# Performance work log

Measured on AMD Instinct MI355X. Metric: run time of the kernel, lower is better.

The kernel has to match this reference:

```python
import jax, jax.numpy as jnp
import numpy as np

B, N_REL, N_OBJ, N_ATT, VOCAB, D = 32, 1024, 1024, 4, 2048, 512


def setup_inputs() -> dict:
    key = jax.random.key(0)
    ks = jax.random.split(key, 12)
    inp = {}
    inp["ssg_rel"] = jax.random.randint(ks[0], (B, N_REL, 3), 0, N_OBJ, dtype=jnp.int32)
    inp["ssg_obj"] = jax.random.randint(ks[1], (B, N_OBJ), 0, VOCAB, dtype=jnp.int32)
    inp["ssg_att"] = jax.random.randint(ks[2], (B, N_OBJ, N_ATT), 0, VOCAB, dtype=jnp.int32)
    inp["emb_table"] = jax.random.normal(ks[3], (VOCAB, D), jnp.float32) * 0.02
    def lin(k, fan_in):
        return jax.random.normal(k, (fan_in, D), jnp.float32) * (1.0 / np.sqrt(fan_in))
    inp["W_sbj"] = lin(ks[4], 3 * D); inp["b_sbj"] = jnp.zeros((D,), jnp.float32)
    inp["W_obj"] = lin(ks[5], 3 * D); inp["b_obj"] = jnp.zeros((D,), jnp.float32)
    inp["W_rel"] = lin(ks[6], 3 * D); inp["b_rel"] = jnp.zeros((D,), jnp.float32)
    inp["W_o"] = lin(ks[7], D);      inp["b_o"] = jnp.zeros((D,), jnp.float32)
    inp["W_a"] = lin(ks[8], 2 * D);  inp["b_a"] = jnp.zeros((D,), jnp.float32)
    return inp


def reference(ssg_rel, ssg_obj, ssg_att, emb_table,
              W_sbj, b_sbj, W_obj, b_obj, W_rel, b_rel, W_o, b_o, W_a, b_a):
    # Dropout is identity in eval mode.
    Bq, N_rel, _ = ssg_rel.shape
    _, N_obj, N_att = ssg_att.shape
    d = emb_table.shape[1]

    rel_mask = (ssg_rel[:, :, 2] == 1)[..., None]      # [B, N_rel, 1], True = pad
    obj_mask = ssg_obj == 1                            # [B, N_obj]
    attr_mask = ssg_att == 1                           # [B, N_obj, N_att]

    rel_emb = emb_table[ssg_rel[:, :, 2]]              # [B, N_rel, d]
    obj_emb = emb_table[ssg_obj]                       # [B, N_obj, d]
    attr_emb = emb_table[ssg_att]                      # [B, N_obj, N_att, d]

    sbj_id = ssg_rel[:, :, 0]
    obj_id = ssg_rel[:, :, 1]
    gather = lambda ids: jnp.take_along_axis(obj_emb, ids[..., None], axis=1)  # [B,N_rel,d]
    sbj_g = gather(sbj_id)
    obj_g = gather(obj_id)

    zfill = lambda x: jnp.where(rel_mask, 0.0, x)
    # Sequential overwriting matches the original: rel_obj/rel_rel use the UPDATED sbj/obj feats.
    sbj_f = zfill(jax.nn.relu(jnp.concatenate([sbj_g, obj_g, rel_emb], -1) @ W_sbj + b_sbj))
    obj_f = zfill(jax.nn.relu(jnp.concatenate([sbj_f, obj_g, rel_emb], -1) @ W_obj + b_obj))
    rel_f = zfill(jax.nn.relu(jnp.concatenate([sbj_f, obj_f, rel_emb], -1) @ W_rel + b_rel))

    node = jnp.where(obj_mask[..., None], 0.0, jax.nn.relu(obj_emb @ W_o + b_o))  # [B,N_obj,d]

    att_in = jnp.concatenate(
        [jnp.broadcast_to(obj_emb[:, :, None, :], (Bq, N_obj, N_att, d)), attr_emb], -1)
    att_f = jnp.where(attr_mask[..., None], 0.0, jax.nn.relu(att_in @ W_a + b_a))  # [B,N_obj,N_att,d]

    bidx = jnp.arange(Bq)[:, None]
    node = node.at[bidx, sbj_id].add(sbj_f)
    node = node.at[bidx, obj_id].add(obj_f)

    # Original builds counts=ones(B, 2*N_rel, N_obj+1) then scatters 1s into it -> a no-op,
    # so counts.sum(dim=1) == 2*N_rel everywhere; the divisor is the constant 2*N_rel.
    rel_object_feat = node / jnp.asarray(2.0 * N_rel, node.dtype)

    att_sum = att_f.sum(axis=2)                        # [B, N_obj, d]
    att_cnt = jnp.sum(~attr_mask, axis=-1)             # [B, N_obj] number of valid attrs
    attr_zero = att_cnt == 0
    denom = jnp.maximum(att_cnt, 1).astype(att_sum.dtype)[..., None]
    att_feat = jnp.where(attr_zero[..., None], 0.0, att_sum / denom)

    ssg_feat = jnp.concatenate([rel_object_feat, rel_f, att_feat], axis=1)
    ssg_mask = jnp.concatenate([obj_mask, rel_mask[..., 0], attr_zero], axis=1)[:, None, None, :]
    return ssg_feat, ssg_mask
```

## Files before the change

kernel.cpp:

```cpp
#include <hip/hip_runtime.h>
#include <hip/hip_bf16.h>

typedef __attribute__((ext_vector_type(8))) short bf16x8;
typedef __attribute__((ext_vector_type(4))) float f32x4;

#define N_OBJ 1024
#define N_REL 1024
#define NB 32
#define D 512
#define VOCAB 2048
#define M_ROWS (NB * N_REL)
#define PRE_BLK (VOCAB * D)
#define WT_BLK (D * D)

__device__ __forceinline__ ushort f2bf(float f) {
    union { float f; unsigned u; } v; v.f = f;
    unsigned u = v.u;
    unsigned r = (u + 0x7FFFu + ((u >> 16) & 1u)) >> 16;
    return (ushort)r;
}
__device__ __forceinline__ float bf2f(ushort h) {
    union { unsigned u; float f; } v; v.u = ((unsigned)h) << 16;
    return v.f;
}

__device__ __forceinline__ void gload16(const ushort* g, const ushort* l) {
    __builtin_amdgcn_global_load_lds(
        (const __attribute__((address_space(1))) void*)(unsigned long long)(const void*)g,
        (__attribute__((address_space(3))) void*)(unsigned)(unsigned long long)(const void*)l,
        16, 0, 0);
}

template <int MODE>
__device__ __forceinline__ void gemm_body(
    int mt, int nt, int q, int tid,
    ushort* __restrict__ sA, ushort* __restrict__ sB,
    const ushort* __restrict__ A, const ushort* __restrict__ WT,
    ushort* __restrict__ PREB,
    const int* __restrict__ ssg_rel, const int* __restrict__ ssg_obj,
    const float* __restrict__ bias,
    ushort* __restrict__ featbuf, float* __restrict__ out0,
    float* __restrict__ out1) {
    const int m0 = mt * 128;
    constexpr int LDA = (MODE == 0) ? 512 : 1024;
    constexpr int KTOT = (MODE == 2) ? 1024 : 512;

    const ushort* BT0;
    const ushort* BT1 = nullptr;
    ushort* PREq = nullptr;
    if (MODE == 0) {
        const int wtq[9] = {0, 1, 2, 4, 5, 8, 9, 10, 11};
        BT0 = WT + (size_t)wtq[q] * WT_BLK + (size_t)nt * 128 * 512;
        PREq = PREB + (size_t)q * PRE_BLK;
    } else if (MODE == 1) {
        BT0 = WT + (size_t)3 * WT_BLK + (size_t)nt * 128 * 512;
    } else {
        BT0 = WT + (size_t)6 * WT_BLK + (size_t)nt * 128 * 512;
        BT1 = WT + (size_t)7 * WT_BLK + (size_t)nt * 128 * 512;
    }

    const int wave = tid >> 6;
    const int wm = wave >> 1, wn = wave & 1;
    const int lr = tid & 15, lk = (tid & 63) >> 4;

    f32x4 acc[4][4];
#pragma unroll
    for (int mi = 0; mi < 4; mi++)
#pragma unroll
        for (int ni = 0; ni < 4; ni++)
            acc[mi][ni] = (f32x4){0.f, 0.f, 0.f, 0.f};

    const ushort* Ag = A + (size_t)m0 * LDA;
    const int srow = tid >> 3;
    const int scol = (tid & 7) * 8;

    for (int k0 = 0; k0 < KTOT; k0 += 64) {
        const ushort* As = Ag + (size_t)srow * LDA + k0 + scol;
        const ushort* Bbase = (MODE == 2 && k0 >= 512) ? (BT1 + (k0 - 512)) : (BT0 + k0);
        const ushort* Bs = Bbase + (size_t)srow * 512 + scol;
#pragma unroll
        for (int i = 0; i < 4; i++)
            gload16(As + (size_t)i * 32 * LDA, &sA[i * 2048 + tid * 8]);
#pragma unroll
        for (int i = 0; i < 4; i++)
            gload16(Bs + (size_t)i * 32 * 512, &sB[i * 2048 + tid * 8]);
        __syncthreads();
#pragma unroll
        for (int ks = 0; ks < 2; ks++) {
            bf16x8 af[4], bfr[4];
#pragma unroll
            for (int mi = 0; mi < 4; mi++)
                af[mi] = *(const bf16x8*)&sA[(wm * 64 + mi * 16 + lr) * 64 + ks * 32 + lk * 8];
#pragma unroll
            for (int ni = 0; ni < 4; ni++)
                bfr[ni] = *(const bf16x8*)&sB[(wn * 64 + ni * 16 + lr) * 64 + ks * 32 + lk * 8];
#pragma unroll
            for (int mi = 0; mi < 4; mi++)
#pragma unroll
                for (int ni = 0; ni < 4; ni++)
                    acc[mi][ni] = __builtin_amdgcn_mfma_f32_16x16x32_bf16(af[mi], bfr[ni], acc[mi][ni], 0, 0, 0);
        }
        __syncthreads();
    }

    int* sIo  = (int*)sA;
    int* sRid = sIo + 128;
    if (MODE == 1 || MODE == 2) {
        if (tid < 128) {
            int R = m0 + tid;
            int rid = ssg_rel[R * 3 + 2];
            sRid[tid] = rid;
            if (MODE == 1) sIo[tid] = ssg_obj[(R & ~(N_OBJ - 1)) + ssg_rel[R * 3 + 1]];
            if (MODE == 2 && nt == 0) {
                int b = R >> 10, rr = R & (N_REL - 1);
                out1[(size_t)b * 3072 + 1024 + rr] = (rid == 1) ? 1.0f : 0.0f;
            }
        }
        __syncthreads();
    }

#pragma unroll
    for (int mi = 0; mi < 4; mi++) {
#pragma unroll
        for (int ni = 0; ni < 4; ni++) {
            int c = wn * 64 + ni * 16 + lr;
            int ch = nt * 128 + c;
#pragma unroll
            for (int j = 0; j < 4; j++) {
                int rl = wm * 64 + mi * 16 + lk * 4 + j;
                int R = m0 + rl;
                float v = acc[mi][ni][j];
                if (MODE == 0) {
                    PREq[(size_t)R * 512 + ch] = f2bf(v);
                } else if (MODE == 1) {
                    int rid = sRid[rl];
                    int io = sIo[rl];
                    float t = v + bf2f(PREB[(size_t)3 * PRE_BLK + (size_t)io * 512 + ch])
                                + bf2f(PREB[(size_t)4 * PRE_BLK + (size_t)rid * 512 + ch])
                                + bias[ch];
                    t = fmaxf(t, 0.f);
                    if (rid == 1) t = 0.f;
                    featbuf[(size_t)R * 1024 + 512 + ch] = f2bf(t);
                } else {
                    int rid = sRid[rl];
                    float t = v + bf2f(PREB[(size_t)5 * PRE_BLK + (size_t)rid * 512 + ch])
                                + bias[ch];
                    t = fmaxf(t, 0.f);
                    if (rid == 1) t = 0.f;
                    int b = R >> 10, rr = R & (N_REL - 1);
                    out0[((size_t)(b * 3072 + 1024 + rr)) * 512 + ch] = t;
                }
            }
        }
    }
}

__global__ __launch_bounds__(256)
void k_setup(const float* __restrict__ E, ushort* __restrict__ EB,
             const float* __restrict__ Wsbj, const float* __restrict__ Wobj,
             const float* __restrict__ Wrel, const float* __restrict__ Wo,
             const float* __restrict__ Wa, ushort* __restrict__ WT,
             int* __restrict__ cnt) {
    int blk = blockIdx.x, tid = threadIdx.x;
    if (blk < 1024) {
        int i = blk * 256 + tid;
        float4 v = ((const float4*)E)[i];
        ushort4 o; o.x = f2bf(v.x); o.y = f2bf(v.y); o.z = f2bf(v.z); o.w = f2bf(v.w);
        ((ushort4*)EB)[i] = o;
    } else if (blk < 4096) {
        __shared__ float s[32][33];
        int bb = blk - 1024;
        int q = bb >> 8, rem = bb & 255;
        int bx = rem & 15, by = rem >> 4;
        const float* src; int ro;
        if (q < 3)       { src = Wsbj; ro = q * 512; }
        else if (q < 6)  { src = Wobj; ro = (q - 3) * 512; }
        else if (q < 9)  { src = Wrel; ro = (q - 6) * 512; }
        else if (q == 9) { src = Wo;   ro = 0; }
        else             { src = Wa;   ro = (q - 10) * 512; }
        int tx = tid & 31, ty = tid >> 5;
        int kbase = by * 32, nbase = bx * 32;
#pragma unroll
        for (int i = 0; i < 4; i++) {
            int k = kbase + ty + i * 8;
            s[ty + i * 8][tx] = src[(size_t)(ro + k) * 512 + nbase + tx];
        }
        __syncthreads();
        ushort* dst = WT + (size_t)q * WT_BLK;
#pragma unroll
        for (int i = 0; i < 4; i++) {
            int n = nbase + ty + i * 8;
            dst[(size_t)n * 512 + kbase + tx] = f2bf(s[tx][ty + i * 8]);
        }
    } else {
        cnt[(blk - 4096) * 256 + tid] = 0;
    }
}

__global__ void k_csr_count(const int* __restrict__ ssg_rel, int* __restrict__ cnt) {
    int r = blockIdx.x * 256 + threadIdx.x;
    int bb = r & ~(N_OBJ - 1);
    atomicAdd(&cnt[bb + ssg_rel[r * 3 + 0]], 1);
    atomicAdd(&cnt[bb + ssg_rel[r * 3 + 1]], 1);
}

__global__ __launch_bounds__(1024)
void k_csr_scan(const int* __restrict__ cnt, int* __restrict__ offs, int* __restrict__ cursor) {
    __shared__ int part[1024];
    int t = threadIdx.x;
    int base = t * 32;
    int local[32];
    int sum = 0;
#pragma unroll
    for (int i = 0; i < 32; i++) { local[i] = sum; sum += cnt[base + i]; }
    part[t] = sum;
    __syncthreads();
    for (int d = 1; d < 1024; d <<= 1) {
        int v = (t >= d) ? part[t - d] : 0;
        __syncthreads();
        part[t] += v;
        __syncthreads();
    }
    int excl = (t == 0) ? 0 : part[t - 1];
#pragma unroll
    for (int i = 0; i < 32; i++) {
        int o = excl + local[i];
        offs[base + i] = o;
        cursor[base + i] = o;
    }
    if (t == 1023) offs[32768] = part[1023];
}

__global__ __launch_bounds__(256)
void k_pre_fill(const ushort* __restrict__ EB, const ushort* __restrict__ WT,
                ushort* __restrict__ PREB, const int* __restrict__ ssg_rel,
                int* __restrict__ cursor, int* __restrict__ lists) {
    int blk = blockIdx.x, tid = threadIdx.x;
    if (blk < 576) {
        int q = blk >> 6, mt = (blk >> 2) & 15, nt = blk & 3;
        if ((q == 2 || q == 4 || q == 5) && mt >= 8) return;
        __shared__ __attribute__((aligned(16))) ushort sA[128 * 64];
        __shared__ __attribute__((aligned(16))) ushort sB[128 * 64];
        gemm_body<0>(mt, nt, q, tid, sA, sB, EB, WT, PREB,
                     nullptr, nullptr, nullptr, nullptr, nullptr, nullptr);
    } else {
        int r = (blk - 576) * 256 + tid;
        int bb = r & ~(N_OBJ - 1);
        int p0 = atomicAdd(&cursor[bb + ssg_rel[r * 3 + 0]], 1);
        lists[p0] = r * 2;
        int p1 = atomicAdd(&cursor[bb + ssg_rel[r * 3 + 1]], 1);
        lists[p1] = r * 2 + 1;
    }
}

__global__ void k_sbj(const int* __restrict__ ssg_rel, const int* __restrict__ ssg_obj,
                      const ushort* __restrict__ PREB, const float* __restrict__ b_sbj,
                      ushort* __restrict__ featbuf) {
    int R = blockIdx.x * 2 + (threadIdx.x >> 7);
    int c4 = threadIdx.x & 127;
    int sid = ssg_rel[R * 3 + 0];
    int oid = ssg_rel[R * 3 + 1];
    int rid = ssg_rel[R * 3 + 2];
    int bb = R & ~(N_OBJ - 1);
    int is_ = ssg_obj[bb + sid];
    int io  = ssg_obj[bb + oid];
    ushort4 p1 = ((const ushort4*)(PREB + (size_t)is_ * 512))[c4];
    ushort4 p2 = ((const ushort4*)(PREB + (size_t)1 * PRE_BLK + (size_t)io * 512))[c4];
    ushort4 p3 = ((const ushort4*)(PREB + (size_t)2 * PRE_BLK + (size_t)rid * 512))[c4];
    float4 b  = ((const float4*)b_sbj)[c4];
    float4 v;
    v.x = fmaxf(bf2f(p1.x) + bf2f(p2.x) + bf2f(p3.x) + b.x, 0.f);
    v.y = fmaxf(bf2f(p1.y) + bf2f(p2.y) + bf2f(p3.y) + b.y, 0.f);
    v.z = fmaxf(bf2f(p1.z) + bf2f(p2.z) + bf2f(p3.z) + b.z, 0.f);
    v.w = fmaxf(bf2f(p1.w) + bf2f(p2.w) + bf2f(p3.w) + b.w, 0.f);
    if (rid == 1) { v.x = v.y = v.z = v.w = 0.f; }
    ushort4 o; o.x = f2bf(v.x); o.y = f2bf(v.y); o.z = f2bf(v.z); o.w = f2bf(v.w);
    *(ushort4*)&featbuf[(size_t)R * 1024 + c4 * 4] = o;
}

__global__ __launch_bounds__(256)
void k_gemm1(const ushort* __restrict__ feat, const ushort* __restrict__ WT,
             ushort* __restrict__ PREB,
             const int* __restrict__ ssg_rel, const int* __restrict__ ssg_obj,
             const float* __restrict__ b_obj, ushort* __restrict__ featbuf) {
    int blk = blockIdx.x;
    int nb = (blk & 7) * 128 + (blk >> 3);
    int mt = nb >> 2, nt = nb & 3;
    __shared__ __attribute__((aligned(16))) ushort sA[128 * 64];
    __shared__ __attribute__((aligned(16))) ushort sB[128 * 64];
    gemm_body<1>(mt, nt, 0, threadIdx.x, sA, sB, feat, WT, PREB,
                 ssg_rel, ssg_obj, b_obj, featbuf, nullptr, nullptr);
}

__global__ __launch_bounds__(256)
void k_gemm2(const ushort* __restrict__ feat, const ushort* __restrict__ WT,
             ushort* __restrict__ PREB,
             const int* __restrict__ ssg_rel, const int* __restrict__ ssg_obj,
             const float* __restrict__ b_rel,
             float* __restrict__ out0, float* __restrict__ out1) {
    int blk = blockIdx.x;
    int nb = (blk & 7) * 128 + (blk >> 3);
    int mt = nb >> 2, nt = nb & 3;
    __shared__ __attribute__((aligned(16))) ushort sA[128 * 64];
    __shared__ __attribute__((aligned(16))) ushort sB[128 * 64];
    gemm_body<2>(mt, nt, 0, threadIdx.x, sA, sB, feat, WT, PREB,
                 ssg_rel, ssg_obj, b_rel, nullptr, out0, out1);
}

__global__ void k_objpass(const int* __restrict__ ssg_obj, const int* __restrict__ ssg_att,
                          const int* __restrict__ offs, const int* __restrict__ lists,
                          const ushort* __restrict__ feat, const ushort* __restrict__ PREB,
                          const float* __restrict__ b_o, const float* __restrict__ b_a,
                          float* __restrict__ out0, float* __restrict__ out1) {
    int Ro = blockIdx.x * 2 + (threadIdx.x >> 7);
    int c4 = threadIdx.x & 127;
    int iv = ssg_obj[Ro];
    int bq = Ro >> 10, o = Ro & (N_OBJ - 1);

    float4 bo4 = ((const float4*)b_o)[c4];
    ushort4 q6 = ((const ushort4*)(PREB + (size_t)6 * PRE_BLK + (size_t)iv * 512))[c4];
    float a0 = 0.f, a1 = 0.f, a2 = 0.f, a3 = 0.f;
    if (iv != 1) {
        a0 = fmaxf(bf2f(q6.x) + bo4.x, 0.f);
        a1 = fmaxf(bf2f(q6.y) + bo4.y, 0.f);
        a2 = fmaxf(bf2f(q6.z) + bo4.z, 0.f);
        a3 = fmaxf(bf2f(q6.w) + bo4.w, 0.f);
    }
    int s = offs[Ro], e = offs[Ro + 1];
    for (int i = s; i < e; ++i) {
        int ent = lists[i];
        ushort4 u = ((const ushort4*)(feat + (size_t)(ent >> 1) * 1024 + (ent & 1) * 512))[c4];
        a0 += bf2f(u.x); a1 += bf2f(u.y); a2 += bf2f(u.z); a3 += bf2f(u.w);
    }
    float4 r;
    r.x = a0 * (1.0f / 2048.0f); r.y = a1 * (1.0f / 2048.0f);
    r.z = a2 * (1.0f / 2048.0f); r.w = a3 * (1.0f / 2048.0f);
    ((float4*)out0)[((size_t)(bq * 3072 + o)) * 128 + c4] = r;

    int j0 = ssg_att[Ro * 4 + 0], j1 = ssg_att[Ro * 4 + 1];
    int j2 = ssg_att[Ro * 4 + 2], j3 = ssg_att[Ro * 4 + 3];
    float4 ba4 = ((const float4*)b_a)[c4];
    ushort4 q7 = ((const ushort4*)(PREB + (size_t)7 * PRE_BLK + (size_t)iv * 512))[c4];
    float bx = bf2f(q7.x) + ba4.x, by = bf2f(q7.y) + ba4.y;
    float bz = bf2f(q7.z) + ba4.z, bw = bf2f(q7.w) + ba4.w;
    int cnt = (j0 != 1) + (j1 != 1) + (j2 != 1) + (j3 != 1);
    float inv = cnt ? 1.0f / (float)cnt : 0.f;
    float sx = 0.f, sy = 0.f, sz = 0.f, sw = 0.f;
    const ushort* A2 = PREB + (size_t)8 * PRE_BLK;
#define ACC_ATT(J) if ((J) != 1) { \
        ushort4 a2 = ((const ushort4*)(A2 + (size_t)(J) * 512))[c4]; \
        sx += fmaxf(bx + bf2f(a2.x), 0.f); sy += fmaxf(by + bf2f(a2.y), 0.f); \
        sz += fmaxf(bz + bf2f(a2.z), 0.f); sw += fmaxf(bw + bf2f(a2.w), 0.f); }
    ACC_ATT(j0) ACC_ATT(j1) ACC_ATT(j2) ACC_ATT(j3)
#undef ACC_ATT
    float4 sv; sv.x = sx * inv; sv.y = sy * inv; sv.z = sz * inv; sv.w = sw * inv;
    ((float4*)out0)[((size_t)(bq * 3072 + 2048 + o)) * 128 + c4] = sv;

    if (c4 == 0) {
        out1[(size_t)bq * 3072 + o] = (iv == 1) ? 1.0f : 0.0f;
        out1[(size_t)bq * 3072 + 2048 + o] = (cnt == 0) ? 1.0f : 0.0f;
    }
}

extern "C" void kernel_launch(void* const* d_in, const int* in_sizes, int n_in,
                              void* d_out, int out_size, void* d_ws, size_t ws_size,
                              hipStream_t stream) {
    const int*   ssg_rel = (const int*)d_in[0];
    const int*   ssg_obj = (const int*)d_in[1];
    const int*   ssg_att = (const int*)d_in[2];
    const float* emb     = (const float*)d_in[3];
    const float* Wsbj    = (const float*)d_in[4];
    const float* bsbj    = (const float*)d_in[5];
    const float* Wobj    = (const float*)d_in[6];
    const float* bobj    = (const float*)d_in[7];
    const float* Wrel    = (const float*)d_in[8];
    const float* brel    = (const float*)d_in[9];
    const float* Wo      = (const float*)d_in[10];
    const float* bo      = (const float*)d_in[11];
    const float* Wa      = (const float*)d_in[12];
    const float* ba      = (const float*)d_in[13];

    float* out0 = (float*)d_out;
    float* out1 = out0 + (size_t)NB * 3072 * 512;

    char* w = (char*)d_ws;
    ushort* EB     = (ushort*)w; w += (size_t)VOCAB * D * 2;
    ushort* WT     = (ushort*)w; w += (size_t)12 * WT_BLK * 2;
    ushort* PREB   = (ushort*)w; w += (size_t)9 * PRE_BLK * 2;
    ushort* feat   = (ushort*)w; w += (size_t)M_ROWS * 1024 * 2;
    int*    cnt    = (int*)   w; w += (size_t)32768 * 4;
    int*    offs   = (int*)   w; w += (size_t)32769 * 4;
    int*    cursor = (int*)   w; w += (size_t)32768 * 4;
    int*    lists  = (int*)   w; w += (size_t)65536 * 4;

    k_setup<<<dim3(4224), dim3(256), 0, stream>>>(emb, EB, Wsbj, Wobj, Wrel, Wo, Wa, WT, cnt);
    k_csr_count<<<dim3(128), dim3(256), 0, stream>>>(ssg_rel, cnt);
    k_csr_scan<<<dim3(1), dim3(1024), 0, stream>>>(cnt, offs, cursor);
    k_pre_fill<<<dim3(704), dim3(256), 0, stream>>>(EB, WT, PREB, ssg_rel, cursor, lists);
    k_sbj<<<dim3(M_ROWS / 2), dim3(256), 0, stream>>>(ssg_rel, ssg_obj, PREB, bsbj, feat);
    k_gemm1<<<dim3(1024), dim3(256), 0, stream>>>(feat, WT, PREB, ssg_rel, ssg_obj, bobj, feat);
    k_gemm2<<<dim3(1024), dim3(256), 0, stream>>>(feat, WT, PREB, ssg_rel, ssg_obj, brel, out0, out1);
    k_objpass<<<dim3(M_ROWS / 2), dim3(256), 0, stream>>>(ssg_obj, ssg_att, offs, lists,
                                                          feat, PREB, bo, ba, out0, out1);
}
```

Measured before the change: 221.0 us.

## Replace relation GEMMs with 256x256-tile, 8-wave, 4-stage pipelined kernel

The two main relation GEMMs (obj-feature and rel-feature) move from 128x128 tiles with 4 waves and a single synchronous LDS buffer to 256x256 tiles with 8 waves, BK=32 and a 4-buffer ring of async global-to-LDS loads kept three stages ahead. Raw ds_read_b128 loads, manual vmcnt waits and s_setprio around the MFMA block are used. The goal is to hide global load latency and raise operand reuse per LDS byte. The cost is fewer blocks (256, about one per CU), higher register pressure from the 8x4 accumulator tiles, and fragile hand-coded wait counts.

```diff
diff --git a/kernel.cpp b/kernel.cpp
--- a/kernel.cpp
+++ b/kernel.cpp
@@ -30,34 +30,24 @@
         (__attribute__((address_space(3))) void*)(unsigned)(unsigned long long)(const void*)l,
         16, 0, 0);
 }
-
-template <int MODE>
-__device__ __forceinline__ void gemm_body(
+__device__ __forceinline__ unsigned lds_off(const void* p) {
+    return (unsigned)(unsigned long long)(const __attribute__((address_space(3))) void*)p;
+}
+__device__ __forceinline__ bf16x8 ds_read128(unsigned off) {
+    bf16x8 r;
+    asm volatile("ds_read_b128 %0, %1" : "=v"(r) : "v"(off));
+    return r;
+}
+
+__device__ __forceinline__ void gemm0_body(
     int mt, int nt, int q, int tid,
     ushort* __restrict__ sA, ushort* __restrict__ sB,
     const ushort* __restrict__ A, const ushort* __restrict__ WT,
-    ushort* __restrict__ PREB,
-    const int* __restrict__ ssg_rel, const int* __restrict__ ssg_obj,
-    const float* __restrict__ bias,
-    ushort* __restrict__ featbuf, float* __restrict__ out0,
-    float* __restrict__ out1) {
+    ushort* __restrict__ PREB) {
     const int m0 = mt * 128;
-    constexpr int LDA = (MODE == 0) ? 512 : 1024;
-    constexpr int KTOT = (MODE == 2) ? 1024 : 512;
-
-    const ushort* BT0;
-    const ushort* BT1 = nullptr;
-    ushort* PREq = nullptr;
-    if (MODE == 0) {
-        const int wtq[9] = {0, 1, 2, 4, 5, 8, 9, 10, 11};
-        BT0 = WT + (size_t)wtq[q] * WT_BLK + (size_t)nt * 128 * 512;
-        PREq = PREB + (size_t)q * PRE_BLK;
-    } else if (MODE == 1) {
-        BT0 = WT + (size_t)3 * WT_BLK + (size_t)nt * 128 * 512;
-    } else {
-        BT0 = WT + (size_t)6 * WT_BLK + (size_t)nt * 128 * 512;
-        BT1 = WT + (size_t)7 * WT_BLK + (size_t)nt * 128 * 512;
-    }
+    const int wtq[9] = {0, 1, 2, 4, 5, 8, 9, 10, 11};
+    const ushort* BT0 = WT + (size_t)wtq[q] * WT_BLK + (size_t)nt * 128 * 512;
+    ushort* PREq = PREB + (size_t)q * PRE_BLK;
 
     const int wave = tid >> 6;
     const int wm = wave >> 1, wn = wave & 1;
@@ -70,17 +60,16 @@
         for (int ni = 0; ni < 4; ni++)
             acc[mi][ni] = (f32x4){0.f, 0.f, 0.f, 0.f};
 
-    const ushort* Ag = A + (size_t)m0 * LDA;
+    const ushort* Ag = A + (size_t)m0 * 512;
     const int srow = tid >> 3;
     const int scol = (tid & 7) * 8;
 
-    for (int k0 = 0; k0 < KTOT; k0 += 64) {
-        const ushort* As = Ag + (size_t)srow * LDA + k0 + scol;
-        const ushort* Bbase = (MODE == 2 && k0 >= 512) ? (BT1 + (k0 - 512)) : (BT0 + k0);
-        const ushort* Bs = Bbase + (size_t)srow * 512 + scol;
+    for (int k0 = 0; k0 < 512; k0 += 64) {
+        const ushort* As = Ag + (size_t)srow * 512 + k0 + scol;
+        const ushort* Bs = BT0 + (size_t)srow * 512 + k0 + scol;
 #pragma unroll
         for (int i = 0; i < 4; i++)
-            gload16(As + (size_t)i * 32 * LDA, &sA[i * 2048 + tid * 8]);
+            gload16(As + (size_t)i * 32 * 512, &sA[i * 2048 + tid * 8]);
 #pragma unroll
         for (int i = 0; i < 4; i++)
             gload16(Bs + (size_t)i * 32 * 512, &sB[i * 2048 + tid * 8]);
@@ -102,37 +91,131 @@
         }
         __syncthreads();
     }
-
-    int* sIo  = (int*)sA;
-    int* sRid = sIo + 128;
-    if (MODE == 1 || MODE == 2) {
-        if (tid < 128) {
-            int R = m0 + tid;
-            int rid = ssg_rel[R * 3 + 2];
-            sRid[tid] = rid;
-            if (MODE == 1) sIo[tid] = ssg_obj[(R & ~(N_OBJ - 1)) + ssg_rel[R * 3 + 1]];
-            if (MODE == 2 && nt == 0) {
-                int b = R >> 10, rr = R & (N_REL - 1);
-                out1[(size_t)b * 3072 + 1024 + rr] = (rid == 1) ? 1.0f : 0.0f;
+#pragma unroll
+    for (int mi = 0; mi < 4; mi++)
+#pragma unroll
+        for (int ni = 0; ni < 4; ni++) {
+            int ch = nt * 128 + wn * 64 + ni * 16 + lr;
+#pragma unroll
+            for (int j = 0; j < 4; j++) {
+                int R = m0 + wm * 64 + mi * 16 + lk * 4 + j;
+                PREq[(size_t)R * 512 + ch] = f2bf(acc[mi][ni][j]);
             }
         }
-        __syncthreads();
-    }
-
-#pragma unroll
-    for (int mi = 0; mi < 4; mi++) {
+}
+
+template <int MODE>
+__global__ __launch_bounds__(512, 2)
+void k_gemm8(const ushort* __restrict__ A, const ushort* __restrict__ WT,
+             const ushort* __restrict__ PREB,
+             const int* __restrict__ ssg_rel, const int* __restrict__ ssg_obj,
+             const float* __restrict__ bias,
+             ushort* __restrict__ featbuf, float* __restrict__ out0,
+             float* __restrict__ out1) {
+    constexpr int KTOT = (MODE == 2) ? 1024 : 512;
+    constexpr int NK = KTOT / 32;
+    constexpr int LDA = 1024;
+    __shared__ __attribute__((aligned(16))) ushort lds[4 * 2 * 256 * 32];
+
+    const int tid = threadIdx.x;
+    int x = blockIdx.x & 7, jj = blockIdx.x >> 3;
+    const int mt = x * 16 + (jj >> 1), nt = jj & 1;
+    const int m0 = mt * 256, n0 = nt * 256;
+
+    const ushort* BT0 = WT + (size_t)((MODE == 1) ? 3 : 6) * WT_BLK + (size_t)n0 * 512;
+    const ushort* BT1 = (MODE == 2) ? (WT + (size_t)7 * WT_BLK + (size_t)n0 * 512) : nullptr;
+
+    const ushort* Ag = A + (size_t)m0 * LDA;
+    const int srow = tid >> 2;
+    const int scol = (tid & 3) * 8;
+
+    const int wave = tid >> 6, lane = tid & 63;
+    const int wm = wave >> 2, wn = wave & 3;
+    const int lr = lane & 15, lk = lane >> 4;
+
+    f32x4 acc[8][4];
+#pragma unroll
+    for (int mi = 0; mi < 8; mi++)
+#pragma unroll
+        for (int ni = 0; ni < 4; ni++)
+            acc[mi][ni] = (f32x4){0.f, 0.f, 0.f, 0.f};
+
+#define STAGE(KT) do {                                                          \
+        int _b = (KT) & 3;                                                      \
+        ushort* _dA = &lds[(_b * 2 + 0) * 8192];                                \
+        ushort* _dB = &lds[(_b * 2 + 1) * 8192];                                \
+        int _k0 = (KT) * 32;                                                    \
+        const ushort* _Bb = (MODE == 2 && _k0 >= 512) ? (BT1 + (_k0 - 512))     \
+                                                      : (BT0 + _k0);            \
+        gload16(Ag + (size_t)(srow) * LDA + _k0 + scol, _dA + srow * 32 + scol);        \
+        gload16(Ag + (size_t)(srow + 128) * LDA + _k0 + scol, _dA + (srow + 128) * 32 + scol); \
+        gload16(_Bb + (size_t)(srow) * 512 + scol, _dB + srow * 32 + scol);             \
+        gload16(_Bb + (size_t)(srow + 128) * 512 + scol, _dB + (srow + 128) * 32 + scol); \
+    } while (0)
+
+    STAGE(0); STAGE(1); STAGE(2);
+
+    for (int kt = 0; kt < NK; ++kt) {
+        if (kt + 3 < NK) {
+            asm volatile("s_waitcnt vmcnt(8)\n\ts_barrier" ::: "memory");
+            STAGE(kt + 3);
+        } else if (kt + 3 == NK) {
+            asm volatile("s_waitcnt vmcnt(8)\n\ts_barrier" ::: "memory");
+        } else if (kt + 2 == NK) {
+            asm volatile("s_waitcnt vmcnt(4)\n\ts_barrier" ::: "memory");
+        } else {
+            asm volatile("s_waitcnt vmcnt(0)\n\ts_barrier" ::: "memory");
+        }
+        {
+            int buf = kt & 3;
+            unsigned baseA = lds_off(&lds[(buf * 2 + 0) * 8192]) + (unsigned)(wm * 128) * 64 + lk * 16;
+            unsigned baseB = lds_off(&lds[(buf * 2 + 1) * 8192]) + (unsigned)(wn * 64) * 64 + lk * 16;
+            bf16x8 bfr[4], af[8];
+#pragma unroll
+            for (int ni = 0; ni < 4; ni++)
+                bfr[ni] = ds_read128(baseB + (unsigned)(ni * 16 + lr) * 64);
+#pragma unroll
+            for (int mi = 0; mi < 8; mi++)
+                af[mi] = ds_read128(baseA + (unsigned)(mi * 16 + lr) * 64);
+            asm volatile("s_waitcnt lgkmcnt(0)" ::: "memory");
+            __builtin_amdgcn_sched_barrier(0);
+            __builtin_amdgcn_s_setprio(1);
+#pragma unroll
+            for (int mi = 0; mi < 8; mi++)
+#pragma unroll
+                for (int ni = 0; ni < 4; ni++)
+                    acc[mi][ni] = __builtin_amdgcn_mfma_f32_16x16x32_bf16(af[mi], bfr[ni], acc[mi][ni], 0, 0, 0);
+            __builtin_amdgcn_s_setprio(0);
+        }
+    }
+#undef STAGE
+
+    __syncthreads();
+    int* sIo  = (int*)lds;
+    int* sRid = sIo + 256;
+    if (tid < 256) {
+        int R = m0 + tid;
+        int rid = ssg_rel[R * 3 + 2];
+        sRid[tid] = rid;
+        if (MODE == 1) sIo[tid] = ssg_obj[(R & ~(N_OBJ - 1)) + ssg_rel[R * 3 + 1]];
+        if (MODE == 2 && nt == 0) {
+            int b = R >> 10, rr = R & (N_REL - 1);
+            out1[(size_t)b * 3072 + 1024 + rr] = (rid == 1) ? 1.0f : 0.0f;
+        }
+    }
+    __syncthreads();
+
+#pragma unroll
+    for (int mi = 0; mi < 8; mi++) {
 #pragma unroll
         for (int ni = 0; ni < 4; ni++) {
-            int c = wn * 64 + ni * 16 + lr;
-            int ch = nt * 128 + c;
+            int ch = n0 + wn * 64 + ni * 16 + lr;
 #pragma unroll
             for (int j = 0; j < 4; j++) {
-                int rl = wm * 64 + mi * 16 + lk * 4 + j;
+                int rl = wm * 128 + mi * 16 + lk * 4 + j;
                 int R = m0 + rl;
                 float v = acc[mi][ni][j];
-                if (MODE == 0) {
-                    PREq[(size_t)R * 512 + ch] = f2bf(v);
-                } else if (MODE == 1) {
+                if (MODE == 1) {
                     int rid = sRid[rl];
                     int io = sIo[rl];
                     float t = v + bf2f(PREB[(size_t)3 * PRE_BLK + (size_t)io * 512 + ch])
@@ -241,8 +324,7 @@
         if ((q == 2 || q == 4 || q == 5) && mt >= 8) return;
         __shared__ __attribute__((aligned(16))) ushort sA[128 * 64];
         __shared__ __attribute__((aligned(16))) ushort sB[128 * 64];
-        gemm_body<0>(mt, nt, q, tid, sA, sB, EB, WT, PREB,
-                     nullptr, nullptr, nullptr, nullptr, nullptr, nullptr);
+        gemm0_body(mt, nt, q, tid, sA, sB, EB, WT, PREB);
     } else {
         int r = (blk - 576) * 256 + tid;
         int bb = r & ~(N_OBJ - 1);
@@ -278,35 +360,6 @@
     *(ushort4*)&featbuf[(size_t)R * 1024 + c4 * 4] = o;
 }
 
-__global__ __launch_bounds__(256)
-void k_gemm1(const ushort* __restrict__ feat, const ushort* __restrict__ WT,
-             ushort* __restrict__ PREB,
-             const int* __restrict__ ssg_rel, const int* __restrict__ ssg_obj,
-             const float* __restrict__ b_obj, ushort* __restrict__ featbuf) {
-    int blk = blockIdx.x;
-    int nb = (blk & 7) * 128 + (blk >> 3);
-    int mt = nb >> 2, nt = nb & 3;
-    __shared__ __attribute__((aligned(16))) ushort sA[128 * 64];
-    __shared__ __attribute__((aligned(16))) ushort sB[128 * 64];
-    gemm_body<1>(mt, nt, 0, threadIdx.x, sA, sB, feat, WT, PREB,
-                 ssg_rel, ssg_obj, b_obj, featbuf, nullptr, nullptr);
-}
-
-__global__ __launch_bounds__(256)
-void k_gemm2(const ushort* __restrict__ feat, const ushort* __restrict__ WT,
-             ushort* __restrict__ PREB,
-             const int* __restrict__ ssg_rel, const int* __restrict__ ssg_obj,
-             const float* __restrict__ b_rel,
-             float* __restrict__ out0, float* __restrict__ out1) {
-    int blk = blockIdx.x;
-    int nb = (blk & 7) * 128 + (blk >> 3);
-    int mt = nb >> 2, nt = nb & 3;
-    __shared__ __attribute__((aligned(16))) ushort sA[128 * 64];
-    __shared__ __attribute__((aligned(16))) ushort sB[128 * 64];
-    gemm_body<2>(mt, nt, 0, threadIdx.x, sA, sB, feat, WT, PREB,
-                 ssg_rel, ssg_obj, b_rel, nullptr, out0, out1);
-}
-
 __global__ void k_objpass(const int* __restrict__ ssg_obj, const int* __restrict__ ssg_att,
                           const int* __restrict__ offs, const int* __restrict__ lists,
                           const ushort* __restrict__ feat, const ushort* __restrict__ PREB,
@@ -398,8 +451,10 @@
     k_csr_scan<<<dim3(1), dim3(1024), 0, stream>>>(cnt, offs, cursor);
     k_pre_fill<<<dim3(704), dim3(256), 0, stream>>>(EB, WT, PREB, ssg_rel, cursor, lists);
     k_sbj<<<dim3(M_ROWS / 2), dim3(256), 0, stream>>>(ssg_rel, ssg_obj, PREB, bsbj, feat);
-    k_gemm1<<<dim3(1024), dim3(256), 0, stream>>>(feat, WT, PREB, ssg_rel, ssg_obj, bobj, feat);
-    k_gemm2<<<dim3(1024), dim3(256), 0, stream>>>(feat, WT, PREB, ssg_rel, ssg_obj, brel, out0, out1);
+    k_gemm8<1><<<dim3(256), dim3(512), 0, stream>>>(feat, WT, PREB, ssg_rel, ssg_obj,
+                                                    bobj, feat, nullptr, nullptr);
+    k_gemm8<2><<<dim3(256), dim3(512), 0, stream>>>(feat, WT, PREB, ssg_rel, ssg_obj,
+                                                    brel, nullptr, out0, out1);
     k_objpass<<<dim3(M_ROWS / 2), dim3(256), 0, stream>>>(ssg_obj, ssg_att, offs, lists,
                                                           feat, PREB, bo, ba, out0, out1);
 }
```

Result: faster. 202.4 us (-8.4%).
